# Kernel tuning notes

Measured on AMD Instinct MI355X. Metric: run time of the kernel, lower is better.

## Reference

```python
import jax, jax.numpy as jnp
import numpy as np

B, C, H = 32, 1000, 512
N = C + 1  # graph nodes = 1 query node + C class nodes
ALPHA_IT = 0.7
BETA_IT = 0.5


def setup_inputs() -> dict:
    key = jax.random.key(0)
    ks = jax.random.split(key, 6)
    stdv = 1.0 / np.sqrt(H)
    return {
        "input_text": jax.random.normal(ks[0], (B, 1, H), jnp.float32),
        "input_img": jax.random.normal(ks[1], (B, 1, H), jnp.float32),
        "base_text_features": jax.random.normal(ks[2], (B, C, H), jnp.float32),
        "base_img_features": jax.random.normal(ks[3], (B, C, H), jnp.float32),
        "W_tt": jax.random.uniform(ks[4], (H, H), jnp.float32, -stdv, stdv),
        "b_tt": jnp.zeros((N, H), jnp.float32),
        "W_it": jax.random.uniform(ks[5], (H, H), jnp.float32, -stdv, stdv),
        "b_it": jnp.zeros((N, H), jnp.float32),
    }


def _cosine_adj(feat):
    # feat: [B, H, N]; F.normalize over dim=1 (feature axis), then x^T x -> [B, N, N]
    xn = feat / jnp.maximum(jnp.linalg.norm(feat, axis=1, keepdims=True), 1e-12)
    return jnp.einsum('bhn,bhm->bnm', xn, xn)


def _gcn(feat, adj, W, b):
    # feat: [B, H, N], adj: [B, N, N]
    adj = jnp.clip(adj, 0.0, None) + jnp.eye(adj.shape[1], dtype=adj.dtype)[None]
    # symmetric norm D^-1/2 A D^-1/2 as a row/col rescale (math-equivalent to diag bmm)
    d = jax.lax.rsqrt(adj.sum(-1))  # [B, N]
    adj = d[:, :, None] * adj * d[:, None, :]
    pre_sup = jnp.einsum('bhn,hk->bnk', feat, W)           # x.T @ W
    out = jnp.einsum('bnm,bmk->bnk', adj, pre_sup) + b[None]
    return jnp.tanh(out[:, 0, :])  # take node 0, apply Tanh -> [B, H]


def reference(input_text, input_img, base_text_features, base_img_features,
              W_tt, b_tt, W_it, b_it):
    # feats built under no_grad + detach in the original
    feat_tt = jax.lax.stop_gradient(
        jnp.concatenate([input_text, base_text_features], axis=1).transpose(0, 2, 1))  # [B,H,N]
    feat_it = jax.lax.stop_gradient(
        jnp.concatenate([input_img, base_img_features], axis=1).transpose(0, 2, 1))
    edge_tt = jax.lax.stop_gradient(_cosine_adj(feat_tt))
    edge_it = jax.lax.stop_gradient(_cosine_adj(feat_it))

    g_tt = _gcn(feat_tt, edge_tt, W_tt, b_tt)  # [B, H]
    g_it = _gcn(feat_it, edge_it, W_it, b_it)
    graph_o = (ALPHA_IT * g_tt + (1.0 - ALPHA_IT) * g_it)[:, None, :]  # [B,1,H]

    out_text = BETA_IT * base_text_features + (1.0 - BETA_IT) * graph_o
    out_img = BETA_IT * base_img_features + (1.0 - BETA_IT) * graph_o
    return (out_text, out_img)
```

## Files before the change

kernel.cpp:

```cpp
#include <hip/hip_runtime.h>
#include <hip/hip_bf16.h>

#define B_ 32
#define C_ 1000
#define H_ 512
#define NP 1024

typedef __attribute__((ext_vector_type(4))) int i32x4;

__device__ __forceinline__ float tanh_fast(float x) {
  float ax = fminf(fabsf(x), 15.0f);
  float e = __expf(2.0f * ax);
  float t = (e - 1.0f) / (e + 1.0f);
  return copysignf(t, x);
}
__device__ __forceinline__ float sc2f(unsigned v) {
  return (float)(int)(signed char)v;
}
__device__ __forceinline__ void gload16(const void* g, void* l) {
  __builtin_amdgcn_global_load_lds((const __attribute__((address_space(1))) unsigned*)g,
                                   (__attribute__((address_space(3))) unsigned*)l, 16, 0, 0);
}

__global__ __launch_bounds__(256) void k_norm(const float* __restrict__ it, const float* __restrict__ ii,
                                              const float* __restrict__ bt, const float* __restrict__ bi,
                                              signed char* __restrict__ xq, float* __restrict__ nrm,
                                              float* __restrict__ qs, float* __restrict__ zero_base) {
  int zi = blockIdx.x * 256 + threadIdx.x;
  if (zi < 114688) zero_base[zi] = 0.0f;

  int u = blockIdx.x;
  int w = threadIdx.x >> 6, lane = threadIdx.x & 63;
  int xcd = u & 7, v = u >> 3;
  int mb = (v & 7) * 8 + xcd;
  int grp = v >> 3;
  int wid = mb * NP + grp * 4 + w;
  int node = grp * 4 + w;
  int b = mb & 31, mod = mb >> 5;
  const float* src = nullptr;
  if (node == 0) src = (mod ? ii : it) + b * H_;
  else if (node <= C_) src = (mod ? bi : bt) + ((size_t)b * C_ + (node - 1)) * H_;
  float4 v0 = make_float4(0.f, 0.f, 0.f, 0.f), v1 = v0;
  if (src) {
    const float4* s4 = (const float4*)src;
    v0 = s4[lane * 2]; v1 = s4[lane * 2 + 1];
  }
  float ss = v0.x*v0.x + v0.y*v0.y + v0.z*v0.z + v0.w*v0.w
           + v1.x*v1.x + v1.y*v1.y + v1.z*v1.z + v1.w*v1.w;
  #pragma unroll
  for (int o = 32; o; o >>= 1) ss += __shfl_xor(ss, o);
  float n = sqrtf(ss);
  if (lane == 0) nrm[wid] = n;
  float inv = 1.0f / fmaxf(n, 1e-12f);
  float x[8] = {v0.x*inv, v0.y*inv, v0.z*inv, v0.w*inv, v1.x*inv, v1.y*inv, v1.z*inv, v1.w*inv};
  float m8 = 0.f;
  #pragma unroll
  for (int j = 0; j < 8; ++j) m8 = fmaxf(m8, fabsf(x[j]));
  #pragma unroll
  for (int o = 32; o; o >>= 1) m8 = fmaxf(m8, __shfl_xor(m8, o));
  if (lane == 0) qs[wid] = m8 * (1.0f / 127.0f);
  float invq = (m8 > 0.f) ? 127.0f / m8 : 0.f;
  int q[8];
  #pragma unroll
  for (int j = 0; j < 8; ++j) q[j] = __float2int_rn(x[j] * invq);
  unsigned lo = (q[0] & 255) | ((q[1] & 255) << 8) | ((q[2] & 255) << 16) | ((unsigned)(q[3] & 255) << 24);
  unsigned hi = (q[4] & 255) | ((q[5] & 255) << 8) | ((q[6] & 255) << 16) | ((unsigned)(q[7] & 255) << 24);
  *(uint2*)(xq + (size_t)wid * H_ + lane * 8) = make_uint2(lo, hi);
}

__global__ __launch_bounds__(256) void k_gram(const signed char* __restrict__ xq,
                                              const float* __restrict__ qs,
                                              float* __restrict__ r, float* __restrict__ sc) {
  __shared__ __align__(16) unsigned char As[3 * 8192];
  __shared__ __align__(16) unsigned char Bs[3 * 8192];
  __shared__ float s_qs[256];
  int orig = blockIdx.x;
  int xcd = orig & 7;
  int k = orig >> 3;
  int mb = xcd + 8 * (k / 36);
  int idx = k % 36;
  int ti = 0, rem = idx;
  while (rem >= 8 - ti) { rem -= 8 - ti; ++ti; }
  int tj = ti + rem;
  bool diag = (ti == tj);
  const signed char* X = xq + (size_t)mb * NP * H_;
  int tid = threadIdx.x;
  int w = tid >> 6, lane = tid & 63;
  int wr = w >> 1, wc = w & 1;

  if (tid < 128) s_qs[tid] = qs[mb * NP + ti * 128 + tid];
  else           s_qs[tid] = qs[mb * NP + tj * 128 + (tid - 128)];

  i32x4 acc[4][4] = {};
  int lrow = lane >> 2;
  int ps0 = lane & 3;

  auto stage = [&](int buf, int ks) {
    #pragma unroll
    for (int q = 0; q < 2; ++q) {
      int chunk = w * 2 + q;
      int row = chunk * 16 + lrow;
      int qq = ps0 ^ ((row >> 1) & 3);
      gload16(X + (size_t)(ti * 128 + row) * H_ + ks * 64 + qq * 16,
              (void*)(As + buf * 8192 + chunk * 1024));
      if (!diag)
        gload16(X + (size_t)(tj * 128 + row) * H_ + ks * 64 + qq * 16,
                (void*)(Bs + buf * 8192 + chunk * 1024));
    }
  };

  auto do_step = [&](const unsigned char* Ab, const unsigned char* Bb) {
    i32x4 af[4], bf[4];
    #pragma unroll
    for (int mi = 0; mi < 4; ++mi) {
      int row = wr * 64 + mi * 16 + (lane & 15);
      int ps = (lane >> 4) ^ ((row >> 1) & 3);
      af[mi] = *(const i32x4*)(Ab + row * 64 + ps * 16);
    }
    #pragma unroll
    for (int ni = 0; ni < 4; ++ni) {
      int row = wc * 64 + ni * 16 + (lane & 15);
      int ps = (lane >> 4) ^ ((row >> 1) & 3);
      bf[ni] = *(const i32x4*)(Bb + row * 64 + ps * 16);
    }
    #pragma unroll
    for (int mi = 0; mi < 4; ++mi)
      #pragma unroll
      for (int ni = 0; ni < 4; ++ni)
        acc[mi][ni] = __builtin_amdgcn_mfma_i32_16x16x64_i8(af[mi], bf[ni], acc[mi][ni], 0, 0, 0);
  };

  stage(0, 0); stage(1, 1); stage(2, 2);
  if (!diag) {
    #pragma unroll
    for (int ks = 0; ks < 8; ++ks) {
      if (ks == 0)      asm volatile("s_waitcnt vmcnt(8)" ::: "memory");
      else if (ks < 7)  asm volatile("s_waitcnt vmcnt(4)" ::: "memory");
      else              asm volatile("s_waitcnt vmcnt(0)" ::: "memory");
      __builtin_amdgcn_s_barrier();
      if (ks >= 1 && ks <= 5) stage((ks + 2) % 3, ks + 2);
      do_step(As + (ks % 3) * 8192, Bs + (ks % 3) * 8192);
    }
  } else {
    #pragma unroll
    for (int ks = 0; ks < 8; ++ks) {
      if (ks == 0)      asm volatile("s_waitcnt vmcnt(4)" ::: "memory");
      else if (ks < 7)  asm volatile("s_waitcnt vmcnt(2)" ::: "memory");
      else              asm volatile("s_waitcnt vmcnt(0)" ::: "memory");
      __builtin_amdgcn_s_barrier();
      if (ks >= 1 && ks <= 5) stage((ks + 2) % 3, ks + 2);
      do_step(As + (ks % 3) * 8192, As + (ks % 3) * 8192);
    }
  }

  __syncthreads();
  float* rr = r + mb * NP;
  float qsc[4];
  #pragma unroll
  for (int ni = 0; ni < 4; ++ni) qsc[ni] = s_qs[128 + wc * 64 + ni * 16 + (lane & 15)];
  #pragma unroll
  for (int mi = 0; mi < 4; ++mi) {
    #pragma unroll
    for (int reg = 0; reg < 4; ++reg) {
      float v = 0.f;
      #pragma unroll
      for (int ni = 0; ni < 4; ++ni) {
        int d = acc[mi][ni][reg];
        v += (d > 0 ? (float)d : 0.f) * qsc[ni];
      }
      v += __shfl_xor(v, 1); v += __shfl_xor(v, 2); v += __shfl_xor(v, 4); v += __shfl_xor(v, 8);
      if ((lane & 15) == 0) {
        int rloc = wr * 64 + mi * 16 + (lane >> 4) * 4 + reg;
        atomicAdd(&rr[ti * 128 + rloc], v * s_qs[rloc]);
      }
    }
  }
  if (!diag) {
    #pragma unroll
    for (int ni = 0; ni < 4; ++ni) {
      float s = 0.f;
      #pragma unroll
      for (int mi = 0; mi < 4; ++mi)
        #pragma unroll
        for (int reg = 0; reg < 4; ++reg) {
          int d = acc[mi][ni][reg];
          s += (d > 0 ? (float)d : 0.f) * s_qs[wr * 64 + mi * 16 + (lane >> 4) * 4 + reg];
        }
      s += __shfl_xor(s, 16); s += __shfl_xor(s, 32);
      if (lane < 16) {
        int cloc = wc * 64 + ni * 16 + lane;
        atomicAdd(&rr[tj * 128 + cloc], s * s_qs[128 + cloc]);
      }
    }
  }
  if (ti == 0 && wr == 0 && (lane >> 4) == 0) {
    float q0 = s_qs[0];
    float* scc = sc + mb * NP;
    #pragma unroll
    for (int ni = 0; ni < 4; ++ni) {
      int col = tj * 128 + wc * 64 + ni * 16 + (lane & 15);
      int d = acc[0][ni][0];
      scc[col] = (d > 0 ? (float)d : 0.f) * q0 * qsc[ni];
    }
  }
}

__global__ __launch_bounds__(256) void k_y(const signed char* __restrict__ xq,
                                           const float* __restrict__ r, const float* __restrict__ sc,
                                           const float* __restrict__ nrm, const float* __restrict__ qs,
                                           float* __restrict__ y) {
  __shared__ float s_w[128];
  __shared__ __align__(16) float s_part[4][512];
  int bid = blockIdx.x;
  int xcd = bid & 7, v = bid >> 3;
  int mb = (v & 7) * 8 + xcd;
  int chunk = v >> 3;
  int m0 = chunk * 128;
  int t = threadIdx.x;
  const float* rr = r + mb * NP;
  if (t < 128) {
    int m = m0 + t;
    float wm = 0.f;
    if (m < 1001) {
      float d0 = rsqrtf(rr[0] + 1.0f);
      float dm = rsqrtf(rr[m] + 1.0f);
      wm = d0 * dm * (sc[mb * NP + m] + (m == 0 ? 1.0f : 0.0f)) * nrm[mb * NP + m] * qs[mb * NP + m];
    }
    s_w[t] = wm;
  }
  __syncthreads();
  int w = t >> 6, lane = t & 63;
  float a[8] = {};
  const signed char* X = xq + (size_t)mb * NP * H_ + lane * 8;
  for (int i = 0; i < 32; ++i) {
    int m = w * 32 + i;
    float wm = s_w[m];
    uint2 vv = *(const uint2*)(X + (size_t)(m0 + m) * H_);
    a[0] = fmaf(wm, sc2f(vv.x), a[0]);
    a[1] = fmaf(wm, sc2f(vv.x >> 8), a[1]);
    a[2] = fmaf(wm, sc2f(vv.x >> 16), a[2]);
    a[3] = fmaf(wm, sc2f(vv.x >> 24), a[3]);
    a[4] = fmaf(wm, sc2f(vv.y), a[4]);
    a[5] = fmaf(wm, sc2f(vv.y >> 8), a[5]);
    a[6] = fmaf(wm, sc2f(vv.y >> 16), a[6]);
    a[7] = fmaf(wm, sc2f(vv.y >> 24), a[7]);
  }
  #pragma unroll
  for (int j = 0; j < 8; ++j) s_part[w][lane * 8 + j] = a[j];
  __syncthreads();
  float v0 = s_part[0][t] + s_part[1][t] + s_part[2][t] + s_part[3][t];
  float v1 = s_part[0][t + 256] + s_part[1][t + 256] + s_part[2][t + 256] + s_part[3][t + 256];
  atomicAdd(&y[mb * H_ + t], v0);
  atomicAdd(&y[mb * H_ + t + 256], v1);
}

__global__ __launch_bounds__(256) void k_go(const float* __restrict__ y,
                                            const float* __restrict__ Wtt, const float* __restrict__ btt,
                                            const float* __restrict__ Wit, const float* __restrict__ bit,
                                            float* __restrict__ go) {
  int bid = blockIdx.x;
  int mb = bid & 63, half = bid >> 6;
  int b = mb & 31, mod = mb >> 5;
  const float* W = mod ? Wit : Wtt;
  const float* bias = mod ? bit : btt;
  float coef = mod ? 0.3f : 0.7f;
  const float* yy = y + mb * H_;
  int k = half * 256 + threadIdx.x;
  float a = bias[k];
  #pragma unroll 8
  for (int h = 0; h < H_; ++h) a = fmaf(yy[h], W[h * H_ + k], a);
  atomicAdd(&go[b * H_ + k], coef * tanh_fast(a));
}

__global__ __launch_bounds__(256) void k_out(const signed char* __restrict__ xq,
                                             const float* __restrict__ nrm, const float* __restrict__ qs,
                                             const float* __restrict__ go, float* __restrict__ out) {
  int u = blockIdx.x;
  int w = threadIdx.x >> 6, lane = threadIdx.x & 63;
  int xcd = u & 7, v = u >> 3;
  int mbix = v / 250;
  int rowgrp = v - mbix * 250;
  int mb = mbix * 8 + xcd;
  int mod = mb >> 5, b = mb & 31;
  int c = rowgrp * 4 + w;
  size_t node_off = (size_t)(mb * NP + c + 1);
  float hnq = 0.5f * nrm[node_off] * qs[node_off];
  uint2 x = *(const uint2*)(xq + node_off * H_ + lane * 8);
  const float4* g4 = (const float4*)(go + b * H_ + lane * 8);
  float4 g0 = g4[0], g1 = g4[1];
  float4 o0, o1;
  o0.x = fmaf(hnq, sc2f(x.x), 0.5f * g0.x);
  o0.y = fmaf(hnq, sc2f(x.x >> 8), 0.5f * g0.y);
  o0.z = fmaf(hnq, sc2f(x.x >> 16), 0.5f * g0.z);
  o0.w = fmaf(hnq, sc2f(x.x >> 24), 0.5f * g0.w);
  o1.x = fmaf(hnq, sc2f(x.y), 0.5f * g1.x);
  o1.y = fmaf(hnq, sc2f(x.y >> 8), 0.5f * g1.y);
  o1.z = fmaf(hnq, sc2f(x.y >> 16), 0.5f * g1.z);
  o1.w = fmaf(hnq, sc2f(x.y >> 24), 0.5f * g1.w);
  size_t orow = (size_t)(mod * 32000 + b * 1000 + c);
  float4* o4 = (float4*)(out + orow * H_ + lane * 8);
  o4[0] = o0; o4[1] = o1;
}

extern "C" void kernel_launch(void* const* d_in, const int* in_sizes, int n_in,
                              void* d_out, int out_size, void* d_ws, size_t ws_size,
                              hipStream_t stream) {
  const float* it  = (const float*)d_in[0];
  const float* ii  = (const float*)d_in[1];
  const float* bt  = (const float*)d_in[2];
  const float* bi  = (const float*)d_in[3];
  const float* Wtt = (const float*)d_in[4];
  const float* btt = (const float*)d_in[5];
  const float* Wit = (const float*)d_in[6];
  const float* bit = (const float*)d_in[7];

  char* ws = (char*)d_ws;
  signed char* xq = (signed char*)ws;
  size_t off = 33554432;
  float* nrm = (float*)(ws + off); off += 262144;
  float* qs  = (float*)(ws + off); off += 262144;
  float* sc  = (float*)(ws + off); off += 262144;
  float* r   = (float*)(ws + off); off += 262144;
  float* y   = (float*)(ws + off); off += 131072;
  float* go  = (float*)(ws + off); off += 65536;

  k_norm<<<16384, 256, 0, stream>>>(it, ii, bt, bi, xq, nrm, qs, r );
  k_gram<<<64 * 36, 256, 0, stream>>>(xq, qs, r, sc);
  k_y<<<512, 256, 0, stream>>>(xq, r, sc, nrm, qs, y);
  k_go<<<128, 256, 0, stream>>>(y, Wtt, btt, Wit, bit, go);
  k_out<<<16000, 256, 0, stream>>>(xq, nrm, qs, go, (float*)d_out);
}
```

Baseline: 127.7 us.

## Fuse y-aggregation and GCN output kernels; deepen gram pipeline to four stages

Merges the weighted node aggregation (k_y) and the W projection plus tanh (k_go) into one kernel with one 512-thread block per batch element. Both modalities are handled in the same block, which removes the y buffer, its zeroing and the atomics on y and go. The gram kernel also moves from triple to quadruple LDS buffering, with vmcnt waits adjusted to match. The fused kernel launches only 32 blocks, so parallelism drops sharply: each block streams about 1 MB of int8 rows and reads both full 512x512 weight matrices serially, which could make it much slower than the 512-block version.

```diff
diff --git a/kernel.cpp b/kernel.cpp
--- a/kernel.cpp
+++ b/kernel.cpp
@@ -27,7 +27,7 @@
                                               signed char* __restrict__ xq, float* __restrict__ nrm,
                                               float* __restrict__ qs, float* __restrict__ zero_base) {
   int zi = blockIdx.x * 256 + threadIdx.x;
-  if (zi < 114688) zero_base[zi] = 0.0f;
+  if (zi < 65536) zero_base[zi] = 0.0f;
 
   int u = blockIdx.x;
   int w = threadIdx.x >> 6, lane = threadIdx.x & 63;
@@ -71,8 +71,8 @@
 __global__ __launch_bounds__(256) void k_gram(const signed char* __restrict__ xq,
                                               const float* __restrict__ qs,
                                               float* __restrict__ r, float* __restrict__ sc) {
-  __shared__ __align__(16) unsigned char As[3 * 8192];
-  __shared__ __align__(16) unsigned char Bs[3 * 8192];
+  __shared__ __align__(16) unsigned char As[4 * 8192];
+  __shared__ __align__(16) unsigned char Bs[4 * 8192];
   __shared__ float s_qs[256];
   int orig = blockIdx.x;
   int xcd = orig & 7;
@@ -130,26 +130,28 @@
         acc[mi][ni] = __builtin_amdgcn_mfma_i32_16x16x64_i8(af[mi], bf[ni], acc[mi][ni], 0, 0, 0);
   };
 
-  stage(0, 0); stage(1, 1); stage(2, 2);
+  stage(0, 0); stage(1, 1); stage(2, 2); stage(3, 3);
   if (!diag) {
     #pragma unroll
     for (int ks = 0; ks < 8; ++ks) {
-      if (ks == 0)      asm volatile("s_waitcnt vmcnt(8)" ::: "memory");
-      else if (ks < 7)  asm volatile("s_waitcnt vmcnt(4)" ::: "memory");
+      if (ks == 0)      asm volatile("s_waitcnt vmcnt(12)" ::: "memory");
+      else if (ks < 6)  asm volatile("s_waitcnt vmcnt(8)" ::: "memory");
+      else if (ks == 6) asm volatile("s_waitcnt vmcnt(4)" ::: "memory");
       else              asm volatile("s_waitcnt vmcnt(0)" ::: "memory");
       __builtin_amdgcn_s_barrier();
-      if (ks >= 1 && ks <= 5) stage((ks + 2) % 3, ks + 2);
-      do_step(As + (ks % 3) * 8192, Bs + (ks % 3) * 8192);
+      if (ks >= 1 && ks <= 4) stage((ks + 3) & 3, ks + 3);
+      do_step(As + (ks & 3) * 8192, Bs + (ks & 3) * 8192);
     }
   } else {
     #pragma unroll
     for (int ks = 0; ks < 8; ++ks) {
-      if (ks == 0)      asm volatile("s_waitcnt vmcnt(4)" ::: "memory");
-      else if (ks < 7)  asm volatile("s_waitcnt vmcnt(2)" ::: "memory");
+      if (ks == 0)      asm volatile("s_waitcnt vmcnt(6)" ::: "memory");
+      else if (ks < 6)  asm volatile("s_waitcnt vmcnt(4)" ::: "memory");
+      else if (ks == 6) asm volatile("s_waitcnt vmcnt(2)" ::: "memory");
       else              asm volatile("s_waitcnt vmcnt(0)" ::: "memory");
       __builtin_amdgcn_s_barrier();
-      if (ks >= 1 && ks <= 5) stage((ks + 2) % 3, ks + 2);
-      do_step(As + (ks % 3) * 8192, As + (ks % 3) * 8192);
+      if (ks >= 1 && ks <= 4) stage((ks + 3) & 3, ks + 3);
+      do_step(As + (ks & 3) * 8192, As + (ks & 3) * 8192);
     }
   }
 
@@ -205,71 +207,66 @@
   }
 }
 
-__global__ __launch_bounds__(256) void k_y(const signed char* __restrict__ xq,
-                                           const float* __restrict__ r, const float* __restrict__ sc,
-                                           const float* __restrict__ nrm, const float* __restrict__ qs,
-                                           float* __restrict__ y) {
-  __shared__ float s_w[128];
-  __shared__ __align__(16) float s_part[4][512];
-  int bid = blockIdx.x;
-  int xcd = bid & 7, v = bid >> 3;
-  int mb = (v & 7) * 8 + xcd;
-  int chunk = v >> 3;
-  int m0 = chunk * 128;
-  int t = threadIdx.x;
-  const float* rr = r + mb * NP;
-  if (t < 128) {
-    int m = m0 + t;
-    float wm = 0.f;
-    if (m < 1001) {
-      float d0 = rsqrtf(rr[0] + 1.0f);
-      float dm = rsqrtf(rr[m] + 1.0f);
-      wm = d0 * dm * (sc[mb * NP + m] + (m == 0 ? 1.0f : 0.0f)) * nrm[mb * NP + m] * qs[mb * NP + m];
-    }
-    s_w[t] = wm;
-  }
-  __syncthreads();
-  int w = t >> 6, lane = t & 63;
-  float a[8] = {};
-  const signed char* X = xq + (size_t)mb * NP * H_ + lane * 8;
-  for (int i = 0; i < 32; ++i) {
-    int m = w * 32 + i;
-    float wm = s_w[m];
-    uint2 vv = *(const uint2*)(X + (size_t)(m0 + m) * H_);
-    a[0] = fmaf(wm, sc2f(vv.x), a[0]);
-    a[1] = fmaf(wm, sc2f(vv.x >> 8), a[1]);
-    a[2] = fmaf(wm, sc2f(vv.x >> 16), a[2]);
-    a[3] = fmaf(wm, sc2f(vv.x >> 24), a[3]);
-    a[4] = fmaf(wm, sc2f(vv.y), a[4]);
-    a[5] = fmaf(wm, sc2f(vv.y >> 8), a[5]);
-    a[6] = fmaf(wm, sc2f(vv.y >> 16), a[6]);
-    a[7] = fmaf(wm, sc2f(vv.y >> 24), a[7]);
-  }
-  #pragma unroll
-  for (int j = 0; j < 8; ++j) s_part[w][lane * 8 + j] = a[j];
-  __syncthreads();
-  float v0 = s_part[0][t] + s_part[1][t] + s_part[2][t] + s_part[3][t];
-  float v1 = s_part[0][t + 256] + s_part[1][t + 256] + s_part[2][t + 256] + s_part[3][t + 256];
-  atomicAdd(&y[mb * H_ + t], v0);
-  atomicAdd(&y[mb * H_ + t + 256], v1);
-}
-
-__global__ __launch_bounds__(256) void k_go(const float* __restrict__ y,
+__global__ __launch_bounds__(512) void k_yg(const signed char* __restrict__ xq,
+                                            const float* __restrict__ r, const float* __restrict__ sc,
+                                            const float* __restrict__ nrm, const float* __restrict__ qs,
                                             const float* __restrict__ Wtt, const float* __restrict__ btt,
                                             const float* __restrict__ Wit, const float* __restrict__ bit,
                                             float* __restrict__ go) {
-  int bid = blockIdx.x;
-  int mb = bid & 63, half = bid >> 6;
-  int b = mb & 31, mod = mb >> 5;
-  const float* W = mod ? Wit : Wtt;
-  const float* bias = mod ? bit : btt;
-  float coef = mod ? 0.3f : 0.7f;
-  const float* yy = y + mb * H_;
-  int k = half * 256 + threadIdx.x;
-  float a = bias[k];
+  __shared__ float s_w[1024];
+  __shared__ __align__(16) float s_part[8][512];
+  __shared__ float ym[2][512];
+  int b = blockIdx.x;
+  int t = threadIdx.x;
+  int w = t >> 6, lane = t & 63;
+
+  for (int mod = 0; mod < 2; ++mod) {
+    int mb = mod * 32 + b;
+    const float* rr = r + mb * NP;
+    __syncthreads();
+    float d0 = rsqrtf(rr[0] + 1.0f);
+    #pragma unroll
+    for (int m = t; m < 1024; m += 512) {
+      float wm = 0.f;
+      if (m < 1001) {
+        float dm = rsqrtf(rr[m] + 1.0f);
+        wm = d0 * dm * (sc[mb * NP + m] + (m == 0 ? 1.0f : 0.0f)) * nrm[mb * NP + m] * qs[mb * NP + m];
+      }
+      s_w[m] = wm;
+    }
+    __syncthreads();
+    float a[8] = {};
+    const signed char* X = xq + (size_t)mb * NP * H_ + (size_t)(w * 128) * H_ + lane * 8;
+    #pragma unroll 8
+    for (int i = 0; i < 128; ++i) {
+      float wm = s_w[w * 128 + i];
+      uint2 vv = *(const uint2*)(X + (size_t)i * H_);
+      a[0] = fmaf(wm, sc2f(vv.x), a[0]);
+      a[1] = fmaf(wm, sc2f(vv.x >> 8), a[1]);
+      a[2] = fmaf(wm, sc2f(vv.x >> 16), a[2]);
+      a[3] = fmaf(wm, sc2f(vv.x >> 24), a[3]);
+      a[4] = fmaf(wm, sc2f(vv.y), a[4]);
+      a[5] = fmaf(wm, sc2f(vv.y >> 8), a[5]);
+      a[6] = fmaf(wm, sc2f(vv.y >> 16), a[6]);
+      a[7] = fmaf(wm, sc2f(vv.y >> 24), a[7]);
+    }
+    #pragma unroll
+    for (int j = 0; j < 8; ++j) s_part[w][lane * 8 + j] = a[j];
+    __syncthreads();
+    float yv = 0.f;
+    #pragma unroll
+    for (int ww = 0; ww < 8; ++ww) yv += s_part[ww][t];
+    ym[mod][t] = yv;
+  }
+  __syncthreads();
+
+  float att = btt[t], ait = bit[t];
   #pragma unroll 8
-  for (int h = 0; h < H_; ++h) a = fmaf(yy[h], W[h * H_ + k], a);
-  atomicAdd(&go[b * H_ + k], coef * tanh_fast(a));
+  for (int h = 0; h < H_; ++h) {
+    att = fmaf(ym[0][h], Wtt[h * H_ + t], att);
+    ait = fmaf(ym[1][h], Wit[h * H_ + t], ait);
+  }
+  go[b * H_ + t] = 0.7f * tanh_fast(att) + 0.3f * tanh_fast(ait);
 }
 
 __global__ __launch_bounds__(256) void k_out(const signed char* __restrict__ xq,
@@ -321,12 +318,10 @@
   float* qs  = (float*)(ws + off); off += 262144;
   float* sc  = (float*)(ws + off); off += 262144;
   float* r   = (float*)(ws + off); off += 262144;
-  float* y   = (float*)(ws + off); off += 131072;
   float* go  = (float*)(ws + off); off += 65536;
 
-  k_norm<<<16384, 256, 0, stream>>>(it, ii, bt, bi, xq, nrm, qs, r );
+  k_norm<<<16384, 256, 0, stream>>>(it, ii, bt, bi, xq, nrm, qs, r);
   k_gram<<<64 * 36, 256, 0, stream>>>(xq, qs, r, sc);
-  k_y<<<512, 256, 0, stream>>>(xq, r, sc, nrm, qs, y);
-  k_go<<<128, 256, 0, stream>>>(y, Wtt, btt, Wit, bit, go);
+  k_yg<<<32, 512, 0, stream>>>(xq, r, sc, nrm, qs, Wtt, btt, Wit, bit, go);
   k_out<<<16000, 256, 0, stream>>>(xq, nrm, qs, go, (float*)d_out);
 }
```

Result: slower. 151.0 us (+18.3%).
